# Kernel tuning notes

Measured on AMD Instinct MI355X. Metric: run time of the kernel, lower is better.

Reference implementation:

```python
import jax, jax.numpy as jnp
import numpy as np

N_NODES = 50000
N_EDGES = 640000
IN_DIM = 4
HIDDEN = 128
N_LAYERS = 4


def _linear_params(key, fan_in, fan_out):
    kw, kb = jax.random.split(key)
    s = 1.0 / jnp.sqrt(jnp.float32(fan_in))
    W = jax.random.uniform(kw, (fan_in, fan_out), jnp.float32, -s, s)
    b = jax.random.uniform(kb, (fan_out,), jnp.float32, -s, s)
    return W, b


def setup_inputs() -> dict:
    key = jax.random.key(0)
    ks = jax.random.split(key, 8)
    x = jax.random.normal(ks[0], (N_NODES, IN_DIM), jnp.float32)
    edge_index = jax.random.randint(ks[1], (2, N_EDGES), 0, N_NODES, dtype=jnp.int64)
    edge_attr = jax.random.uniform(ks[2], (N_EDGES, 1), jnp.float32)

    W_enc, b_enc = _linear_params(ks[3], IN_DIM, HIDDEN)

    # Per-layer message MLP: Linear(2H+1, H) -> ReLU -> Linear(H, H)
    W1s, b1s, W2s, b2s = [], [], [], []
    lkeys = jax.random.split(ks[4], N_LAYERS)
    for lk in lkeys:
        k1, k2 = jax.random.split(lk)
        W1, b1 = _linear_params(k1, 2 * HIDDEN + 1, HIDDEN)
        W2, b2 = _linear_params(k2, HIDDEN, HIDDEN)
        W1s.append(W1); b1s.append(b1); W2s.append(W2); b2s.append(b2)
    W1 = jnp.stack(W1s); b1 = jnp.stack(b1s)
    W2 = jnp.stack(W2s); b2 = jnp.stack(b2s)

    W_ghost, b_ghost = _linear_params(ks[5], HIDDEN, 1)
    W_period, b_period = _linear_params(ks[6], HIDDEN, 1)
    W_grad, b_grad = _linear_params(ks[7], HIDDEN, 2)

    return {
        "x": x, "edge_index": edge_index, "edge_attr": edge_attr,
        "W_enc": W_enc, "b_enc": b_enc,
        "W1": W1, "b1": b1, "W2": W2, "b2": b2,
        "W_ghost": W_ghost, "b_ghost": b_ghost,
        "W_period": W_period, "b_period": b_period,
        "W_grad": W_grad, "b_grad": b_grad,
    }


def reference(x, edge_index, edge_attr, W_enc, b_enc, W1, b1, W2, b2,
              W_ghost, b_ghost, W_period, b_period, W_grad, b_grad):
    # PyG: x_j = source = edge_index[0], x_i = target = edge_index[1]; aggr='add' at target.
    src = edge_index[0]
    dst = edge_index[1]

    h = x @ W_enc + b_enc  # [N, H]
    for l in range(N_LAYERS):
        # gather -> concat [x_i, x_j, edge_attr] -> 2-layer MLP -> scatter-add
        flow = jnp.concatenate([h[dst], h[src], edge_attr], axis=-1)  # [E, 2H+1]
        msg = jnp.maximum(flow @ W1[l] + b1[l], 0.0) @ W2[l] + b2[l]  # [E, H]
        agg = jax.ops.segment_sum(msg, dst, num_segments=N_NODES)    # [N, H]
        h = jnp.maximum(agg, 0.0)

    ghost_score = jax.nn.sigmoid(h @ W_ghost + b_ghost)  # [N, 1]
    period_pred = h @ W_period + b_period                # [N, 1]
    grad_pred = h @ W_grad + b_grad                      # [N, 2]
    # Note: ghost_locations/ghost_periods in the original are a data-dependent
    # boolean-mask select (not jit-compatible); the mask is derivable from
    # ghost_score/grad_pred, so we return the dense tensors that define it.
    return (h, ghost_score, period_pred, grad_pred)
```

## Files before the change

### kernel.cpp

```cpp
#include <hip/hip_runtime.h>
#include <hip/hip_fp16.h>

#define N_NODES 50000
#define N_EDGES 640000
#define HIDDEN  128
#define N_LAYERS 4
#define TILE_E  128
#define EBLK    (N_EDGES / TILE_E)
#define NCHUNK  196
#define NBLK64  ((N_NODES + 63) / 64)

#define OUT_GHOST  (N_NODES * HIDDEN)
#define OUT_PERIOD (OUT_GHOST + N_NODES)
#define OUT_GRAD   (OUT_PERIOD + N_NODES)

typedef _Float16 f16x8 __attribute__((ext_vector_type(8)));
typedef _Float16 f16x2 __attribute__((ext_vector_type(2)));
typedef float    f32x4 __attribute__((ext_vector_type(4)));

__device__ __forceinline__ int swz(int row, int colbyte) {
    return (row * 256 + colbyte) ^ ((row & 7) << 4);
}

__device__ __forceinline__ int ei_is64(const int* __restrict__ ei) {
    return (ei[1] == 0 && ei[3] == 0 && ei[5] == 0) ? 1 : 0;
}
__device__ __forceinline__ int ei_src(const int* __restrict__ ei, int is64, int e) {
    return is64 ? ei[2 * e] : ei[e];
}
__device__ __forceinline__ int ei_dst(const int* __restrict__ ei, int is64, int e) {
    return is64 ? ei[2 * (N_EDGES + e)] : ei[N_EDGES + e];
}

__global__ void count_kernel(const int* __restrict__ ei, int* __restrict__ counts) {
    int e = blockIdx.x * 256 + threadIdx.x;
    atomicAdd(&counts[ei_dst(ei, ei_is64(ei), e)], 1);
}

__global__ void chunk_reduce_kernel(const int* __restrict__ counts, int* __restrict__ chunkSum) {
    __shared__ int sdata[256];
    int t = threadIdx.x, i = blockIdx.x * 256 + t;
    sdata[t] = (i < N_NODES) ? counts[i] : 0;
    __syncthreads();
    for (int off = 128; off > 0; off >>= 1) {
        if (t < off) sdata[t] += sdata[t + off];
        __syncthreads();
    }
    if (t == 0) chunkSum[blockIdx.x] = sdata[0];
}

__global__ void chunk_scan_kernel(const int* __restrict__ chunkSum, int* __restrict__ chunkBase) {
    __shared__ int buf[256];
    int t = threadIdx.x;
    int v = (t < NCHUNK) ? chunkSum[t] : 0;
    buf[t] = v;
    __syncthreads();
    for (int off = 1; off < 256; off <<= 1) {
        int add = (t >= off) ? buf[t - off] : 0;
        __syncthreads();
        buf[t] += add;
        __syncthreads();
    }
    if (t < NCHUNK) chunkBase[t] = buf[t] - v;
}

__global__ void cursor_kernel(const int* __restrict__ counts, const int* __restrict__ chunkBase,
                              int* __restrict__ cursor) {
    __shared__ int buf[256];
    int t = threadIdx.x, i = blockIdx.x * 256 + t;
    int v = (i < N_NODES) ? counts[i] : 0;
    buf[t] = v;
    __syncthreads();
    for (int off = 1; off < 256; off <<= 1) {
        int add = (t >= off) ? buf[t - off] : 0;
        __syncthreads();
        buf[t] += add;
        __syncthreads();
    }
    if (i < N_NODES) cursor[i] = chunkBase[blockIdx.x] + buf[t] - v;
}

__global__ void scatter_kernel(const int* __restrict__ ei, const float* __restrict__ ea,
                               int* __restrict__ cursor,
                               unsigned int* __restrict__ sdP, _Float16* __restrict__ eaP) {
    int e = blockIdx.x * 256 + threadIdx.x;
    int is64 = ei_is64(ei);
    int s = ei_src(ei, is64, e);
    int d = ei_dst(ei, is64, e);
    int p = atomicAdd(&cursor[d], 1);
    sdP[p] = (unsigned)s | ((unsigned)d << 16);
    eaP[p] = (_Float16)ea[e];
}

__global__ void pack_w_kernel(const float* __restrict__ W1, const float* __restrict__ W2,
                              _Float16* __restrict__ W1c, _Float16* __restrict__ W2p) {
    int id = blockIdx.x * 256 + threadIdx.x;
    if (id < 131072) {
        int j = id & 7, l = (id >> 3) & 63, c = (id >> 9) & 15, kb = (id >> 13) & 3, lay = id >> 15;
        int k = kb * 32 + (l >> 4) * 8 + j, col = c * 16 + (l & 15);
        const float* Wl = W1 + (size_t)lay * 257 * 128;
        W1c[id] = (_Float16)((col < 128) ? Wl[(size_t)k * 128 + col]
                                         : Wl[(size_t)(128 + k) * 128 + (col - 128)]);
    } else if (id < 196608) {
        int id2 = id - 131072;
        int j = id2 & 7, l = (id2 >> 3) & 63, c = (id2 >> 9) & 7, kb = (id2 >> 12) & 3, lay = id2 >> 14;
        int k = kb * 32 + (l >> 4) * 8 + j, col = c * 16 + (l & 15);
        W2p[id2] = (_Float16)W2[(size_t)lay * 128 * 128 + (size_t)k * 128 + col];
    }
}

__global__ void node_init_kernel(const int* __restrict__ counts, int* __restrict__ bslot,
                                 _Float16* __restrict__ aggH) {
    int n = blockIdx.x * 256 + threadIdx.x;
    if (n < N_NODES) {
        bslot[n] = -1;
        if (counts[n] == 0) {
            float4 z = {0.f, 0.f, 0.f, 0.f};
#pragma unroll
            for (int i = 0; i < 16; ++i)
                *(float4*)&aggH[(size_t)n * 128 + i * 8] = z;
        }
    }
}

__global__ void bnd_setup_kernel(const unsigned int* __restrict__ sdP, int* __restrict__ bslot) {
    int t = blockIdx.x * 256 + threadIdx.x;
    if (t >= 1 && t < EBLK) {
        unsigned dp = sdP[t * TILE_E - 1] >> 16;
        unsigned d0 = sdP[t * TILE_E] >> 16;
        if (dp == d0) bslot[d0] = t;
    }
}

__global__ __launch_bounds__(512, 8)
void edge_gather_kernel(const _Float16* __restrict__ PQ,
                        const unsigned int* __restrict__ sdP,
                        const _Float16* __restrict__ eaP,
                        const float* __restrict__ w1last,
                        _Float16* __restrict__ aggH, float* __restrict__ agg32c) {
    __shared__ __align__(16) unsigned char tile[TILE_E * 256];
    __shared__ int dstL[TILE_E];
    __shared__ int srcL[TILE_E];
    __shared__ _Float16 eaL[TILE_E];
    __shared__ int segStart[TILE_E + 1];
    __shared__ int nsegS, contP, contN;

    const int tid = threadIdx.x;
    const int bid = (blockIdx.x & 7) * (EBLK / 8) + (blockIdx.x >> 3);
    const int e_base = bid * TILE_E;

    if (tid < TILE_E) {
        unsigned u = sdP[e_base + tid];
        srcL[tid] = (int)(u & 0xFFFFu);
        dstL[tid] = (int)(u >> 16);
        eaL[tid]  = eaP[e_base + tid];
    } else if (tid == TILE_E) {
        contP = (e_base > 0 && (sdP[e_base - 1] >> 16) == (sdP[e_base] >> 16)) ? 1 : 0;
    } else if (tid == TILE_E + 1) {
        contN = (e_base + TILE_E < N_EDGES &&
                 (sdP[e_base + TILE_E - 1] >> 16) == (sdP[e_base + TILE_E] >> 16)) ? 1 : 0;
    }
    __syncthreads();

    if (tid < 128) {
        int lane = tid & 63;
        int fl_lo = (lane == 0) ? 1 : (dstL[lane] != dstL[lane - 1]);
        unsigned long long m0 = __ballot(fl_lo);
        if (tid < 64) {
            if (fl_lo) segStart[__popcll(m0 & ((1ull << lane) - 1))] = lane;
        } else {
            int j = 64 + lane;
            int fl = (dstL[j] != dstL[j - 1]);
            unsigned long long m1 = __ballot(fl);
            int nlo = __popcll(m0);
            if (fl) segStart[nlo + __popcll(m1 & ((1ull << lane) - 1))] = j;
            if (lane == 0) {
                int ns = nlo + __popcll(m1);
                nsegS = ns;
                segStart[ns] = TILE_E;
            }
        }
    }

    {
        const int t16 = tid & 15, rg = tid >> 4;
        const int c8 = t16 * 8;

        f16x8 pv[4], qv[4];
#pragma unroll
        for (int rr = 0; rr < 4; ++rr) {
            int row = rg + 32 * rr;
            pv[rr] = *(const f16x8*)&PQ[(size_t)dstL[row] * 256 + c8];
            qv[rr] = *(const f16x8*)&PQ[(size_t)srcL[row] * 256 + 128 + c8];
        }

        f16x8 wl8, z8;
#pragma unroll
        for (int j = 0; j < 8; ++j) {
            wl8[j] = (_Float16)w1last[c8 + j];
            z8[j]  = (_Float16)0.f;
        }

#pragma unroll
        for (int rr = 0; rr < 4; ++rr) {
            int row = rg + 32 * rr;
            f16x8 t = pv[rr] + qv[rr] + wl8 * eaL[row];
            f16x8 hv = __builtin_elementwise_max(t, z8);
            *(f16x8*)(tile + swz(row, c8 * 2)) = hv;
        }
    }
    __syncthreads();

    {
        int col2 = (tid & 63) * 2, sh = tid >> 6;
        int ns = nsegS, cP = contP, cN = contN;
        for (int s = sh; s < ns; s += 8) {
            int b = segStart[s], en = segStart[s + 1];
            float s0 = 0.f, s1 = 0.f;
            for (int e2 = b; e2 < en; ++e2) {
                f16x2 hv = *(const f16x2*)(tile + swz(e2, col2 * 2));
                s0 += (float)hv[0];
                s1 += (float)hv[1];
            }
            bool isP = (s == 0 && cP), isN = (s == ns - 1 && cN);
            if (isP || isN) {
                int slot = isP ? bid : bid + 1;
                atomicAdd(&agg32c[(size_t)slot * 128 + col2], s0);
                atomicAdd(&agg32c[(size_t)slot * 128 + col2 + 1], s1);
            } else {
                int node = dstL[b];
                f16x2 o; o[0] = (_Float16)s0; o[1] = (_Float16)s1;
                *(f16x2*)&aggH[(size_t)node * 128 + col2] = o;
            }
        }
    }
}

__global__ __launch_bounds__(512, 6)
void node_layer_kernel(const _Float16* __restrict__ aggH,
                       const int* __restrict__ counts,
                       const int* __restrict__ bslot, float* __restrict__ agg32c,
                       const _Float16* __restrict__ W2p, const float* __restrict__ b2,
                       const _Float16* __restrict__ W1c, const float* __restrict__ b1n,
                       _Float16* __restrict__ PQ, float* __restrict__ out,
                       const float* __restrict__ Wg, const float* __restrict__ bg,
                       const float* __restrict__ Wp, const float* __restrict__ bp,
                       const float* __restrict__ Wr, const float* __restrict__ br,
                       int last) {
    __shared__ __align__(16) unsigned char tile[64 * 256];
    __shared__ int degL[64];
    __shared__ float hw[512];

    const int tid = threadIdx.x;
    const int base = blockIdx.x * 64;

    {
        const int t16 = tid & 15, rg = tid >> 4;
#pragma unroll
        for (int rr = 0; rr < 2; ++rr) {
            int row = rg + 32 * rr;
            int n = base + row;
            f16x8 v = {0, 0, 0, 0, 0, 0, 0, 0};
            if (n < N_NODES) {
                int bs = bslot[n];
                if (bs >= 0) {
                    float* ap = &agg32c[(size_t)bs * 128 + t16 * 8];
                    float4 a = *(const float4*)ap;
                    float4 b = *(const float4*)(ap + 4);
                    v[0] = (_Float16)a.x; v[1] = (_Float16)a.y;
                    v[2] = (_Float16)a.z; v[3] = (_Float16)a.w;
                    v[4] = (_Float16)b.x; v[5] = (_Float16)b.y;
                    v[6] = (_Float16)b.z; v[7] = (_Float16)b.w;
                    float4 z = {0.f, 0.f, 0.f, 0.f};
                    *(float4*)ap = z; *(float4*)(ap + 4) = z;
                } else {
                    v = *(const f16x8*)&aggH[(size_t)n * 128 + t16 * 8];
                }
            }
            *(f16x8*)(tile + swz(row, t16 * 16)) = v;
        }
        if (tid < 64) degL[tid] = (base + tid < N_NODES) ? counts[base + tid] : 0;
        if (last) {
            if (tid < 128)       hw[tid] = Wg[tid];
            else if (tid < 256)  hw[tid] = Wp[tid - 128];
            else                 hw[tid] = Wr[tid - 256];
        }
    }
    __syncthreads();

    const int w = tid >> 6, l = tid & 63, l16 = l & 15, lg = l >> 4;

    f32x4 acc[4];
#pragma unroll
    for (int rt = 0; rt < 4; ++rt) acc[rt] = (f32x4){0.f, 0.f, 0.f, 0.f};
    const f16x8* W2v = (const f16x8*)W2p;
#pragma unroll
    for (int kb = 0; kb < 4; ++kb) {
        f16x8 bf = W2v[(kb * 8 + w) * 64 + l];
#pragma unroll
        for (int rt = 0; rt < 4; ++rt) {
            f16x8 a = *(const f16x8*)(tile + swz(rt * 16 + l16, kb * 64 + lg * 16));
            acc[rt] = __builtin_amdgcn_mfma_f32_16x16x32_f16(a, bf, acc[rt], 0, 0, 0);
        }
    }
    __syncthreads();

    {
        int col = 16 * w + l16;
        float bias = b2[col];
#pragma unroll
        for (int rt = 0; rt < 4; ++rt)
#pragma unroll
            for (int r = 0; r < 4; ++r) {
                int row = rt * 16 + lg * 4 + r;
                float h = fmaxf(acc[rt][r] + (float)degL[row] * bias, 0.f);
                *(_Float16*)(tile + swz(row, col * 2)) = (_Float16)h;
                if (last && base + row < N_NODES)
                    out[(size_t)(base + row) * 128 + col] = h;
            }
    }
    __syncthreads();

    if (last) {
        int r = tid >> 3, part = tid & 7;
        float sg = 0.f, sp = 0.f, s0 = 0.f, s1 = 0.f;
#pragma unroll
        for (int i = 0; i < 8; ++i) {
            int c = part * 16 + i * 2;
            f16x2 hv = *(const f16x2*)(tile + swz(r, c * 2));
            float h0 = (float)hv[0], h1 = (float)hv[1];
            sg += h0 * hw[c] + h1 * hw[c + 1];
            sp += h0 * hw[128 + c] + h1 * hw[128 + c + 1];
            s0 += h0 * hw[256 + c * 2] + h1 * hw[256 + (c + 1) * 2];
            s1 += h0 * hw[256 + c * 2 + 1] + h1 * hw[256 + (c + 1) * 2 + 1];
        }
        sg += __shfl_xor(sg, 1); sg += __shfl_xor(sg, 2); sg += __shfl_xor(sg, 4);
        sp += __shfl_xor(sp, 1); sp += __shfl_xor(sp, 2); sp += __shfl_xor(sp, 4);
        s0 += __shfl_xor(s0, 1); s0 += __shfl_xor(s0, 2); s0 += __shfl_xor(s0, 4);
        s1 += __shfl_xor(s1, 1); s1 += __shfl_xor(s1, 2); s1 += __shfl_xor(s1, 4);
        int n = base + r;
        if (part == 0 && n < N_NODES) {
            float g = sg + bg[0];
            out[OUT_GHOST + n]        = 1.f / (1.f + expf(-g));
            out[OUT_PERIOD + n]       = sp + bp[0];
            out[OUT_GRAD + n * 2]     = s0 + br[0];
            out[OUT_GRAD + n * 2 + 1] = s1 + br[1];
        }
        return;
    }

    f32x4 acc2[2][4];
#pragma unroll
    for (int ci = 0; ci < 2; ++ci)
#pragma unroll
        for (int rt = 0; rt < 4; ++rt) acc2[ci][rt] = (f32x4){0.f, 0.f, 0.f, 0.f};
    const f16x8* W1v = (const f16x8*)W1c;
#pragma unroll
    for (int kb = 0; kb < 4; ++kb) {
        f16x8 b0  = W1v[(kb * 16 + 2 * w) * 64 + l];
        f16x8 b1f = W1v[(kb * 16 + 2 * w + 1) * 64 + l];
#pragma unroll
        for (int rt = 0; rt < 4; ++rt) {
            f16x8 a = *(const f16x8*)(tile + swz(rt * 16 + l16, kb * 64 + lg * 16));
            acc2[0][rt] = __builtin_amdgcn_mfma_f32_16x16x32_f16(a, b0,  acc2[0][rt], 0, 0, 0);
            acc2[1][rt] = __builtin_amdgcn_mfma_f32_16x16x32_f16(a, b1f, acc2[1][rt], 0, 0, 0);
        }
    }
#pragma unroll
    for (int ci = 0; ci < 2; ++ci) {
        int col = (2 * w + ci) * 16 + l16;
        float bb = (col < 128) ? b1n[col] : 0.f;
#pragma unroll
        for (int rt = 0; rt < 4; ++rt)
#pragma unroll
            for (int r = 0; r < 4; ++r) {
                int row = rt * 16 + lg * 4 + r;
                if (base + row < N_NODES)
                    PQ[(size_t)(base + row) * 256 + col] = (_Float16)(acc2[ci][rt][r] + bb);
            }
    }
}

__global__ __launch_bounds__(512, 6)
void node_enc_kernel(const float* __restrict__ x,
                     const float* __restrict__ Wenc, const float* __restrict__ benc,
                     const _Float16* __restrict__ W1c, const float* __restrict__ b1n,
                     _Float16* __restrict__ PQ) {
    __shared__ __align__(16) unsigned char tile[64 * 256];
    const int tid = threadIdx.x;
    const int base = blockIdx.x * 64;

    {
        const int t16 = tid & 15, rg = tid >> 4;
        const int c8 = t16 * 8;
        float wv[4][8], bv[8];
#pragma unroll
        for (int i = 0; i < 4; ++i) {
            float4 a = *(const float4*)&Wenc[i * 128 + c8];
            float4 b = *(const float4*)&Wenc[i * 128 + c8 + 4];
            wv[i][0] = a.x; wv[i][1] = a.y; wv[i][2] = a.z; wv[i][3] = a.w;
            wv[i][4] = b.x; wv[i][5] = b.y; wv[i][6] = b.z; wv[i][7] = b.w;
        }
        float4 ba = *(const float4*)&benc[c8];
        float4 bb = *(const float4*)&benc[c8 + 4];
        bv[0] = ba.x; bv[1] = ba.y; bv[2] = ba.z; bv[3] = ba.w;
        bv[4] = bb.x; bv[5] = bb.y; bv[6] = bb.z; bv[7] = bb.w;
#pragma unroll
        for (int rr = 0; rr < 2; ++rr) {
            int row = rg + 32 * rr;
            float4 xr = {0.f, 0.f, 0.f, 0.f};
            if (base + row < N_NODES) xr = *(const float4*)&x[(size_t)(base + row) * 4];
            f16x8 hv;
#pragma unroll
            for (int j = 0; j < 8; ++j) {
                float v = bv[j] + xr.x * wv[0][j] + xr.y * wv[1][j] + xr.z * wv[2][j] + xr.w * wv[3][j];
                hv[j] = (_Float16)v;
            }
            *(f16x8*)(tile + swz(row, c8 * 2)) = hv;
        }
    }
    __syncthreads();

    const int w = tid >> 6, l = tid & 63, l16 = l & 15, lg = l >> 4;
    f32x4 acc2[2][4];
#pragma unroll
    for (int ci = 0; ci < 2; ++ci)
#pragma unroll
        for (int rt = 0; rt < 4; ++rt) acc2[ci][rt] = (f32x4){0.f, 0.f, 0.f, 0.f};
    const f16x8* W1v = (const f16x8*)W1c;
#pragma unroll
    for (int kb = 0; kb < 4; ++kb) {
        f16x8 b0  = W1v[(kb * 16 + 2 * w) * 64 + l];
        f16x8 b1f = W1v[(kb * 16 + 2 * w + 1) * 64 + l];
#pragma unroll
        for (int rt = 0; rt < 4; ++rt) {
            f16x8 a = *(const f16x8*)(tile + swz(rt * 16 + l16, kb * 64 + lg * 16));
            acc2[0][rt] = __builtin_amdgcn_mfma_f32_16x16x32_f16(a, b0,  acc2[0][rt], 0, 0, 0);
            acc2[1][rt] = __builtin_amdgcn_mfma_f32_16x16x32_f16(a, b1f, acc2[1][rt], 0, 0, 0);
        }
    }
#pragma unroll
    for (int ci = 0; ci < 2; ++ci) {
        int col = (2 * w + ci) * 16 + l16;
        float bb = (col < 128) ? b1n[col] : 0.f;
#pragma unroll
        for (int rt = 0; rt < 4; ++rt)
#pragma unroll
            for (int r = 0; r < 4; ++r) {
                int row = rt * 16 + lg * 4 + r;
                if (base + row < N_NODES)
                    PQ[(size_t)(base + row) * 256 + col] = (_Float16)(acc2[ci][rt][r] + bb);
            }
    }
}

extern "C" void kernel_launch(void* const* d_in, const int* in_sizes, int n_in,
                              void* d_out, int out_size, void* d_ws, size_t ws_size,
                              hipStream_t stream) {
    const float* x     = (const float*)d_in[0];
    const int*   ei    = (const int*)d_in[1];
    const float* ea    = (const float*)d_in[2];
    const float* W_enc = (const float*)d_in[3];
    const float* b_enc = (const float*)d_in[4];
    const float* W1    = (const float*)d_in[5];
    const float* b1    = (const float*)d_in[6];
    const float* W2    = (const float*)d_in[7];
    const float* b2    = (const float*)d_in[8];
    const float* Wg    = (const float*)d_in[9];
    const float* bg    = (const float*)d_in[10];
    const float* Wp    = (const float*)d_in[11];
    const float* bp    = (const float*)d_in[12];
    const float* Wr    = (const float*)d_in[13];
    const float* br    = (const float*)d_in[14];

    float* out = (float*)d_out;

    char* ws = (char*)d_ws;
    _Float16*     PQ     = (_Float16*)ws;     ws += (size_t)N_NODES * 256 * 2;
    _Float16*     aggH   = (_Float16*)ws;     ws += (size_t)N_NODES * 128 * 2;
    float*        agg32c = (float*)ws;        ws += (size_t)EBLK * 128 * 4;
    unsigned int* sdP    = (unsigned int*)ws; ws += (size_t)N_EDGES * 4;
    _Float16*     eaP    = (_Float16*)ws;     ws += (size_t)N_EDGES * 2;
    int*          counts = (int*)ws;          ws += 200192;
    int*          cursor = (int*)ws;          ws += 200192;
    int*          bslot  = (int*)ws;          ws += 200192;
    _Float16*     W1c    = (_Float16*)ws;     ws += (size_t)131072 * 2;
    _Float16*     W2p    = (_Float16*)ws;     ws += (size_t)65536 * 2;
    int*          chunkSum  = (int*)ws;       ws += 1024;
    int*          chunkBase = (int*)ws;       ws += 1024;

    hipMemsetAsync(counts, 0, (size_t)N_NODES * 4, stream);
    hipMemsetAsync(agg32c, 0, (size_t)EBLK * 128 * 4, stream);

    count_kernel<<<N_EDGES / 256, 256, 0, stream>>>(ei, counts);
    chunk_reduce_kernel<<<NCHUNK, 256, 0, stream>>>(counts, chunkSum);
    chunk_scan_kernel<<<1, 256, 0, stream>>>(chunkSum, chunkBase);
    cursor_kernel<<<NCHUNK, 256, 0, stream>>>(counts, chunkBase, cursor);
    scatter_kernel<<<N_EDGES / 256, 256, 0, stream>>>(ei, ea, cursor, sdP, eaP);

    pack_w_kernel<<<196608 / 256, 256, 0, stream>>>(W1, W2, W1c, W2p);
    node_init_kernel<<<NCHUNK, 256, 0, stream>>>(counts, bslot, aggH);
    bnd_setup_kernel<<<(EBLK + 255) / 256, 256, 0, stream>>>(sdP, bslot);

    node_enc_kernel<<<NBLK64, 512, 0, stream>>>(x, W_enc, b_enc, W1c, b1, PQ);

    for (int l = 0; l < N_LAYERS; ++l) {
        edge_gather_kernel<<<EBLK, 512, 0, stream>>>(
            PQ, sdP, eaP,
            W1 + (size_t)l * 257 * 128 + 256 * 128,
            aggH, agg32c);
        int nl = (l < 3) ? (l + 1) : 0;
        node_layer_kernel<<<NBLK64, 512, 0, stream>>>(
            aggH, counts, bslot, agg32c,
            W2p + (size_t)l * 16384, b2 + l * HIDDEN,
            W1c + (size_t)nl * 32768, b1 + nl * HIDDEN,
            PQ, out, Wg, bg, Wp, bp, Wr, br,
            (l == N_LAYERS - 1) ? 1 : 0);
    }
}
```

Before: 314.2 us.

## Fuse CSR setup kernels and pack edge src/dst/attr into one uint2 stream

Merges the chunk reduce, local scan and node-init kernels into a single csr_local kernel and folds the chunk base offset into the scatter step, which drops two launches. Edge src/dst and the fp32 edge attribute are stored together as one uint2 per edge. The gather kernel now loads them directly into registers and issues the PQ row gathers before the shared-memory setup and barrier, so the dependent gathers start earlier. In exchange the edge stream grows from 6 to 8 bytes per edge, and dstL is still read a second time for the segment logic.

Measured after the change: 322.3 us. 1.03x slower.

```diff
diff --git a/kernel.cpp b/kernel.cpp
--- a/kernel.cpp
+++ b/kernel.cpp
@@ -37,16 +37,31 @@
     atomicAdd(&counts[ei_dst(ei, ei_is64(ei), e)], 1);
 }
 
-__global__ void chunk_reduce_kernel(const int* __restrict__ counts, int* __restrict__ chunkSum) {
-    __shared__ int sdata[256];
+__global__ void csr_local_kernel(const int* __restrict__ counts, int* __restrict__ cursor,
+                                 int* __restrict__ chunkSum, int* __restrict__ bslot,
+                                 _Float16* __restrict__ aggH) {
+    __shared__ int buf[256];
     int t = threadIdx.x, i = blockIdx.x * 256 + t;
-    sdata[t] = (i < N_NODES) ? counts[i] : 0;
-    __syncthreads();
-    for (int off = 128; off > 0; off >>= 1) {
-        if (t < off) sdata[t] += sdata[t + off];
+    int v = (i < N_NODES) ? counts[i] : 0;
+    buf[t] = v;
+    __syncthreads();
+    for (int off = 1; off < 256; off <<= 1) {
+        int add = (t >= off) ? buf[t - off] : 0;
         __syncthreads();
-    }
-    if (t == 0) chunkSum[blockIdx.x] = sdata[0];
+        buf[t] += add;
+        __syncthreads();
+    }
+    if (i < N_NODES) {
+        cursor[i] = buf[t] - v;
+        bslot[i] = -1;
+        if (v == 0) {
+            float4 z = {0.f, 0.f, 0.f, 0.f};
+#pragma unroll
+            for (int k = 0; k < 16; ++k)
+                *(float4*)&aggH[(size_t)i * 128 + k * 8] = z;
+        }
+    }
+    if (t == 255) chunkSum[blockIdx.x] = buf[255];
 }
 
 __global__ void chunk_scan_kernel(const int* __restrict__ chunkSum, int* __restrict__ chunkBase) {
@@ -64,32 +79,18 @@
     if (t < NCHUNK) chunkBase[t] = buf[t] - v;
 }
 
-__global__ void cursor_kernel(const int* __restrict__ counts, const int* __restrict__ chunkBase,
-                              int* __restrict__ cursor) {
-    __shared__ int buf[256];
-    int t = threadIdx.x, i = blockIdx.x * 256 + t;
-    int v = (i < N_NODES) ? counts[i] : 0;
-    buf[t] = v;
-    __syncthreads();
-    for (int off = 1; off < 256; off <<= 1) {
-        int add = (t >= off) ? buf[t - off] : 0;
-        __syncthreads();
-        buf[t] += add;
-        __syncthreads();
-    }
-    if (i < N_NODES) cursor[i] = chunkBase[blockIdx.x] + buf[t] - v;
-}
-
 __global__ void scatter_kernel(const int* __restrict__ ei, const float* __restrict__ ea,
-                               int* __restrict__ cursor,
-                               unsigned int* __restrict__ sdP, _Float16* __restrict__ eaP) {
+                               const int* __restrict__ chunkBase, int* __restrict__ cursor,
+                               uint2* __restrict__ sdPE) {
     int e = blockIdx.x * 256 + threadIdx.x;
     int is64 = ei_is64(ei);
     int s = ei_src(ei, is64, e);
     int d = ei_dst(ei, is64, e);
-    int p = atomicAdd(&cursor[d], 1);
-    sdP[p] = (unsigned)s | ((unsigned)d << 16);
-    eaP[p] = (_Float16)ea[e];
+    int p = chunkBase[d >> 8] + atomicAdd(&cursor[d], 1);
+    uint2 v;
+    v.x = (unsigned)s | ((unsigned)d << 16);
+    v.y = __float_as_uint(ea[e]);
+    sdPE[p] = v;
 }
 
 __global__ void pack_w_kernel(const float* __restrict__ W1, const float* __restrict__ W2,
@@ -109,39 +110,22 @@
     }
 }
 
-__global__ void node_init_kernel(const int* __restrict__ counts, int* __restrict__ bslot,
-                                 _Float16* __restrict__ aggH) {
-    int n = blockIdx.x * 256 + threadIdx.x;
-    if (n < N_NODES) {
-        bslot[n] = -1;
-        if (counts[n] == 0) {
-            float4 z = {0.f, 0.f, 0.f, 0.f};
-#pragma unroll
-            for (int i = 0; i < 16; ++i)
-                *(float4*)&aggH[(size_t)n * 128 + i * 8] = z;
-        }
-    }
-}
-
-__global__ void bnd_setup_kernel(const unsigned int* __restrict__ sdP, int* __restrict__ bslot) {
+__global__ void bnd_setup_kernel(const uint2* __restrict__ sdPE, int* __restrict__ bslot) {
     int t = blockIdx.x * 256 + threadIdx.x;
     if (t >= 1 && t < EBLK) {
-        unsigned dp = sdP[t * TILE_E - 1] >> 16;
-        unsigned d0 = sdP[t * TILE_E] >> 16;
+        unsigned dp = sdPE[t * TILE_E - 1].x >> 16;
+        unsigned d0 = sdPE[t * TILE_E].x >> 16;
         if (dp == d0) bslot[d0] = t;
     }
 }
 
 __global__ __launch_bounds__(512, 8)
 void edge_gather_kernel(const _Float16* __restrict__ PQ,
-                        const unsigned int* __restrict__ sdP,
-                        const _Float16* __restrict__ eaP,
+                        const uint2* __restrict__ sdPE,
                         const float* __restrict__ w1last,
                         _Float16* __restrict__ aggH, float* __restrict__ agg32c) {
     __shared__ __align__(16) unsigned char tile[TILE_E * 256];
     __shared__ int dstL[TILE_E];
-    __shared__ int srcL[TILE_E];
-    __shared__ _Float16 eaL[TILE_E];
     __shared__ int segStart[TILE_E + 1];
     __shared__ int nsegS, contP, contN;
 
@@ -149,16 +133,28 @@
     const int bid = (blockIdx.x & 7) * (EBLK / 8) + (blockIdx.x >> 3);
     const int e_base = bid * TILE_E;
 
+    const int t16 = tid & 15, rg = tid >> 4;
+    const int c8 = t16 * 8;
+    uint2 sd[4];
+#pragma unroll
+    for (int rr = 0; rr < 4; ++rr) sd[rr] = sdPE[e_base + rg + 32 * rr];
+
+    f16x8 pv[4], qv[4];
+#pragma unroll
+    for (int rr = 0; rr < 4; ++rr) {
+        int s = (int)(sd[rr].x & 0xFFFFu);
+        int d = (int)(sd[rr].x >> 16);
+        pv[rr] = *(const f16x8*)&PQ[(size_t)d * 256 + c8];
+        qv[rr] = *(const f16x8*)&PQ[(size_t)s * 256 + 128 + c8];
+    }
+
     if (tid < TILE_E) {
-        unsigned u = sdP[e_base + tid];
-        srcL[tid] = (int)(u & 0xFFFFu);
-        dstL[tid] = (int)(u >> 16);
-        eaL[tid]  = eaP[e_base + tid];
+        dstL[tid] = (int)(sdPE[e_base + tid].x >> 16);
     } else if (tid == TILE_E) {
-        contP = (e_base > 0 && (sdP[e_base - 1] >> 16) == (sdP[e_base] >> 16)) ? 1 : 0;
+        contP = (e_base > 0 && (sdPE[e_base - 1].x >> 16) == (sdPE[e_base].x >> 16)) ? 1 : 0;
     } else if (tid == TILE_E + 1) {
         contN = (e_base + TILE_E < N_EDGES &&
-                 (sdP[e_base + TILE_E - 1] >> 16) == (sdP[e_base + TILE_E] >> 16)) ? 1 : 0;
+                 (sdPE[e_base + TILE_E - 1].x >> 16) == (sdPE[e_base + TILE_E].x >> 16)) ? 1 : 0;
     }
     __syncthreads();
 
@@ -183,28 +179,17 @@
     }
 
     {
-        const int t16 = tid & 15, rg = tid >> 4;
-        const int c8 = t16 * 8;
-
-        f16x8 pv[4], qv[4];
-#pragma unroll
-        for (int rr = 0; rr < 4; ++rr) {
-            int row = rg + 32 * rr;
-            pv[rr] = *(const f16x8*)&PQ[(size_t)dstL[row] * 256 + c8];
-            qv[rr] = *(const f16x8*)&PQ[(size_t)srcL[row] * 256 + 128 + c8];
-        }
-
         f16x8 wl8, z8;
 #pragma unroll
         for (int j = 0; j < 8; ++j) {
             wl8[j] = (_Float16)w1last[c8 + j];
             z8[j]  = (_Float16)0.f;
         }
-
 #pragma unroll
         for (int rr = 0; rr < 4; ++rr) {
             int row = rg + 32 * rr;
-            f16x8 t = pv[rr] + qv[rr] + wl8 * eaL[row];
+            _Float16 ea16 = (_Float16)__uint_as_float(sd[rr].y);
+            f16x8 t = pv[rr] + qv[rr] + wl8 * ea16;
             f16x8 hv = __builtin_elementwise_max(t, z8);
             *(f16x8*)(tile + swz(row, c8 * 2)) = hv;
         }
@@ -479,8 +464,7 @@
     _Float16*     PQ     = (_Float16*)ws;     ws += (size_t)N_NODES * 256 * 2;
     _Float16*     aggH   = (_Float16*)ws;     ws += (size_t)N_NODES * 128 * 2;
     float*        agg32c = (float*)ws;        ws += (size_t)EBLK * 128 * 4;
-    unsigned int* sdP    = (unsigned int*)ws; ws += (size_t)N_EDGES * 4;
-    _Float16*     eaP    = (_Float16*)ws;     ws += (size_t)N_EDGES * 2;
+    uint2*        sdPE   = (uint2*)ws;        ws += (size_t)N_EDGES * 8;
     int*          counts = (int*)ws;          ws += 200192;
     int*          cursor = (int*)ws;          ws += 200192;
     int*          bslot  = (int*)ws;          ws += 200192;
@@ -493,20 +477,18 @@
     hipMemsetAsync(agg32c, 0, (size_t)EBLK * 128 * 4, stream);
 
     count_kernel<<<N_EDGES / 256, 256, 0, stream>>>(ei, counts);
-    chunk_reduce_kernel<<<NCHUNK, 256, 0, stream>>>(counts, chunkSum);
+    csr_local_kernel<<<NCHUNK, 256, 0, stream>>>(counts, cursor, chunkSum, bslot, aggH);
     chunk_scan_kernel<<<1, 256, 0, stream>>>(chunkSum, chunkBase);
-    cursor_kernel<<<NCHUNK, 256, 0, stream>>>(counts, chunkBase, cursor);
-    scatter_kernel<<<N_EDGES / 256, 256, 0, stream>>>(ei, ea, cursor, sdP, eaP);
+    scatter_kernel<<<N_EDGES / 256, 256, 0, stream>>>(ei, ea, chunkBase, cursor, sdPE);
 
     pack_w_kernel<<<196608 / 256, 256, 0, stream>>>(W1, W2, W1c, W2p);
-    node_init_kernel<<<NCHUNK, 256, 0, stream>>>(counts, bslot, aggH);
-    bnd_setup_kernel<<<(EBLK + 255) / 256, 256, 0, stream>>>(sdP, bslot);
+    bnd_setup_kernel<<<(EBLK + 255) / 256, 256, 0, stream>>>(sdPE, bslot);
 
     node_enc_kernel<<<NBLK64, 512, 0, stream>>>(x, W_enc, b_enc, W1c, b1, PQ);
 
     for (int l = 0; l < N_LAYERS; ++l) {
         edge_gather_kernel<<<EBLK, 512, 0, stream>>>(
-            PQ, sdP, eaP,
+            PQ, sdPE,
             W1 + (size_t)l * 257 * 128 + 256 * 128,
             aggH, agg32c);
         int nl = (l < 3) ? (l + 1) : 0;
```
